# Kernel tuning notes

Measured on AMD Instinct MI355X. Metric: run time of the kernel, lower is better.

Reference implementation:

```python
import jax, jax.numpy as jnp
import numpy as np
from jax import lax

B, L, D, F, K = 16, 1024, 384, 1536, 3
MAX_DUR = 10          # clamp on per-token duration (makes output length static)
T_OUT = L * MAX_DUR   # padded expanded length
ALPHA = 1.0
EPS = 1e-5


def conv1d_same(x_ncl, w, b):
    # x_ncl: [B, Cin, L], w: [Cout, Cin, K]
    y = lax.conv_general_dilated(x_ncl, w, window_strides=(1,), padding='SAME',
                                 dimension_numbers=('NCH', 'OIH', 'NCH'))
    return y + b[None, :, None]


def conv_block(x, wA, bA, wB, bB):
    # x: [B, L, D] -> Conv(D->F) ReLU Conv(F->D) ReLU -> [B, L, D]
    h = x.transpose(0, 2, 1)
    h = jax.nn.relu(conv1d_same(h, wA, bA))
    h = jax.nn.relu(conv1d_same(h, wB, bB))
    return h.transpose(0, 2, 1)


def layernorm(x, g, b):
    mu = jnp.mean(x, axis=-1, keepdims=True)
    var = jnp.var(x, axis=-1, keepdims=True)
    return (x - mu) * lax.rsqrt(var + EPS) * g + b


def setup_inputs() -> dict:
    key = jax.random.key(0)
    ks = jax.random.split(key, 8)
    s = 0.02
    return {
        'y': jax.random.normal(ks[0], (B, L, D), jnp.float32),
        'token_lengths': jax.random.randint(ks[1], (B,), 1, L + 1).astype(jnp.int32),
        'w1a': jax.random.normal(ks[2], (F, D, K), jnp.float32) * s,
        'b1a': jnp.zeros((F,), jnp.float32),
        'w1b': jax.random.normal(ks[3], (D, F, K), jnp.float32) * s,
        'b1b': jnp.zeros((D,), jnp.float32),
        'g1': jnp.ones((D,), jnp.float32),
        'be1': jnp.zeros((D,), jnp.float32),
        'w2a': jax.random.normal(ks[4], (F, D, K), jnp.float32) * s,
        'b2a': jnp.zeros((F,), jnp.float32),
        'w2b': jax.random.normal(ks[5], (D, F, K), jnp.float32) * s,
        'b2b': jnp.zeros((D,), jnp.float32),
        'g2': jnp.ones((D,), jnp.float32),
        'be2': jnp.zeros((D,), jnp.float32),
        'wl': jax.random.normal(ks[6], (D, 1), jnp.float32) * s,
        'bl': jnp.zeros((1,), jnp.float32),
    }


def reference(y, token_lengths, w1a, b1a, w1b, b1b, g1, be1,
              w2a, b2a, w2b, b2b, g2, be2, wl, bl):
    # DurationPredictor (eval mode: dropout is identity)
    h = conv_block(y, w1a, b1a, w1b, b1b)
    h = layernorm(h, g1, be1)
    h = conv_block(h, w2a, b2a, w2b, b2b)
    h = layernorm(h, g2, be2)
    preds = h @ wl + bl                      # [B, L, 1]

    # lengths = round(alpha * exp(preds)), masked to valid tokens, clamped
    lns = jnp.round(ALPHA * jnp.exp(preds[..., 0]))
    lns = jnp.clip(lns, 0, MAX_DUR).astype(jnp.int32)        # [B, L]
    mask = jnp.arange(L)[None, :] < token_lengths[:, None]
    lns = jnp.where(mask, lns, 0)

    # ragged repeat_interleave + pad, fully vectorized:
    # output frame t maps to token idx = searchsorted(cumsum(lns), t, 'right')
    csum = jnp.cumsum(lns, axis=1)                            # [B, L]
    totals = csum[:, -1]                                      # [B]
    t = jnp.arange(T_OUT, dtype=jnp.int32)
    idx = jax.vmap(lambda c: jnp.searchsorted(c, t, side='right'))(csum)  # [B, T_OUT]
    idx = jnp.minimum(idx, L - 1)
    gathered = jnp.take_along_axis(y, idx[..., None], axis=1)  # [B, T_OUT, D]
    valid = t[None, :] < totals[:, None]
    enlarged = jnp.where(valid[..., None], gathered, 0.0)
    return enlarged, totals
```

## Files before the change

kernel.cpp:

```cpp
#include <hip/hip_runtime.h>
#include <hip/hip_bf16.h>

#define BB 16
#define LL 1024
#define DD 384
#define FF 1536
#define KK 3
#define T_OUT 10240
#define MAX_DUR 10

#define PADL 1026
#define LO_SCALE 2048.0f
#define LO_INV   4.8828125e-4f

typedef _Float16 f16x8 __attribute__((ext_vector_type(8)));
typedef float    f32x4 __attribute__((ext_vector_type(4)));

__device__ __forceinline__ void gll16(const void* g, void* l) {
    __builtin_amdgcn_global_load_lds(
        (const __attribute__((address_space(1))) void*)g,
        (__attribute__((address_space(3))) void*)l, 16, 0, 0);
}

__device__ __forceinline__ void split_write(float v, _Float16* hi, _Float16* lo, size_t off) {
    _Float16 h = (_Float16)v;
    hi[off] = h;
    lo[off] = (_Float16)((v - (float)h) * LO_SCALE);
}

__device__ __forceinline__ float split_read(const _Float16* hi, const _Float16* lo, size_t off) {
    return (float)hi[off] + (float)lo[off] * LO_INV;
}

__global__ void wfrag_k(const float* __restrict__ w, _Float16* __restrict__ hi,
                        _Float16* __restrict__ lo, int O, int I) {
    int id = blockIdx.x * 256 + threadIdx.x;
    int total = O * 3 * I;
    if (id >= total) return;
    int e = id & 7;
    int lane = (id >> 3) & 63;
    int rest = id >> 9;
    int nKT = (3 * I) >> 5;
    int ktl = rest % nKT;
    int ot = rest / nKT;
    int o = ot * 16 + (lane & 15);
    int koff = ((lane >> 4) << 3) + e;
    int kseg = ktl % 3;
    int i = (ktl / 3) * 32 + koff;
    float v = w[(o * I + i) * 3 + kseg];
    split_write(v, hi, lo, id);
}

__global__ void ysplit_k(const float* __restrict__ y, _Float16* __restrict__ hi,
                         _Float16* __restrict__ lo) {
    int id = blockIdx.x * 256 + threadIdx.x;
    if (id >= BB * PADL * DD) return;
    int d = id % DD;
    int r = id / DD;
    int b = r / PADL;
    int lr = r - b * PADL;
    float v = 0.f;
    if (lr >= 1 && lr <= LL) v = y[((size_t)(b << 10) + (lr - 1)) * DD + d];
    split_write(v, hi, lo, id);
}

__global__ void padzero_k(_Float16* __restrict__ hi, _Float16* __restrict__ lo, int width) {
    int id = blockIdx.x * 256 + threadIdx.x;
    if (id >= BB * 2 * width) return;
    int b = id / (2 * width);
    int rem = id - b * 2 * width;
    int row = (rem / width) ? (PADL - 1) : 0;
    int c = rem % width;
    size_t off = (size_t)(b * PADL + row) * width + c;
    hi[off] = (_Float16)0.f;
    lo[off] = (_Float16)0.f;
}

template<int MI, int BN, int OCC, int CIN, int COUT, int KTOT, int NN>
__global__ __launch_bounds__(256, OCC) void gemm_split(
        const _Float16* __restrict__ Ahi, const _Float16* __restrict__ Alo,
        const _Float16* __restrict__ WfH, const _Float16* __restrict__ WfL,
        const float* __restrict__ bias,
        _Float16* __restrict__ Ohi, _Float16* __restrict__ Olo) {
    constexpr int BM   = MI * 32;
    constexpr int AC   = (BM + 2) * 4;
    constexpr int AC4  = AC / 4;
    constexpr int AIT  = (AC4 + 63) / 64;
    constexpr int NA   = 2 * AIT;
    constexpr int AHH  = AC * 8;
    constexpr int ABH  = 4 * AHH;
    constexpr int SEGS = BN / 16;
    constexpr int QS   = SEGS / 4;
    constexpr int NB   = 2 * QS;
    constexpr int JJ   = BN / 32;
    constexpr int BBH  = 2 * BN * 32;
    constexpr int KEEP0  = NB;
    constexpr int KEEP12 = NA + NB;
    constexpr int nKT = KTOT >> 5;
    constexpr int nJ  = nKT / 3;
    __shared__ __align__(16) _Float16 lds_h[ABH + 2 * BBH];
    const int tid = threadIdx.x;
    const int lane = tid & 63;
    const int w = tid >> 6;
    const int lm = lane & 15, lq = lane >> 4;
    const int xcd = blockIdx.x & 7;
    const int t2 = blockIdx.x >> 3;
    const int g  = t2 / (4 * NN);
    const int r  = t2 - g * (4 * NN);
    const int n_t = r >> 2;
    const int mi  = r & 3;
    const int m_t = ((g * 4 + mi) << 3) + xcd;
    const int m0 = m_t * BM;
    const int n0 = n_t * BN;
    const int b = m0 >> 10;
    const int l0 = m0 & 1023;
    const int rowBase = b * PADL + l0;
    const int wm = (w >> 1) * (MI * 16), wn = (w & 1) * (BN / 2);

    f32x4 accM[MI][JJ], accC[MI][JJ];
    const f32x4 zz = {0.f, 0.f, 0.f, 0.f};
    #pragma unroll
    for (int i = 0; i < MI; ++i)
        #pragma unroll
        for (int jj = 0; jj < JJ; ++jj) { accM[i][jj] = zz; accC[i][jj] = zz; }

    int aRowK[AIT];
    bool aAct[AIT];
    #pragma unroll
    for (int it = 0; it < AIT; ++it) {
        int cl = it * 64 + lane;
        int s  = w * AC4 + cl;
        int p = s >> 3, sl = s & 7;
        int t = sl ^ (p & 7);
        int m = p * 2 + (t >> 2);
        int k8 = t & 3;
        aRowK[it] = (rowBase + m) * CIN + k8 * 8;
        aAct[it] = (cl < AC4);
    }
    int bBase[QS];
    #pragma unroll
    for (int q = 0; q < QS; ++q) {
        int ntg = (n0 >> 4) + w * QS + q;
        bBase[q] = (ntg * nKT * 64 + lane) * 8;
    }

    auto stageA = [&](int jt, int bidx) {
        int d0 = jt << 5;
        _Float16* abase = lds_h + bidx * (2 * AHH);
        #pragma unroll
        for (int it = 0; it < AIT; ++it) {
            size_t aoff = (size_t)(unsigned)(aRowK[it] + d0);
            _Float16* hb = abase + (w * AC4 + it * 64) * 8;
            if (aAct[it]) {
                gll16(Ahi + aoff, hb);
                gll16(Alo + aoff, hb + AHH);
            }
        }
    };

    auto stageB = [&](int kt, int bidx) {
        int ktc = kt < nKT ? kt : nKT - 1;
        _Float16* bb = lds_h + ABH + bidx * BBH;
        #pragma unroll
        for (int q = 0; q < QS; ++q) {
            int sg = w * QS + q;
            size_t boff = (size_t)(unsigned)(bBase[q] + ktc * 512);
            gll16(WfH + boff, bb + sg * 512);
            gll16(WfL + boff, bb + BN * 32 + sg * 512);
        }
    };

    auto compute = [&](const _Float16* ab, const _Float16* bb, int kseg) {
        f16x8 bH[JJ], bL[JJ];
        #pragma unroll
        for (int jj = 0; jj < JJ; ++jj) {
            int nl = (w & 1) * JJ + jj;
            bH[jj] = *(const f16x8*)(bb + nl * 512 + lane * 8);
            bL[jj] = *(const f16x8*)(bb + BN * 32 + nl * 512 + lane * 8);
        }
        __builtin_amdgcn_s_setprio(1);
        #pragma unroll
        for (int i = 0; i < MI; ++i) {
            int row = wm + i * 16 + lm + kseg;
            int p = row >> 1;
            int sl = (((row & 1) << 2) | lq) ^ (p & 7);
            int off = p * 64 + sl * 8;
            f16x8 aH = *(const f16x8*)(ab + off);
            f16x8 aL = *(const f16x8*)(ab + AHH + off);
            #pragma unroll
            for (int jj = 0; jj < JJ; ++jj) {
                accM[i][jj] = __builtin_amdgcn_mfma_f32_16x16x32_f16(aH, bH[jj], accM[i][jj], 0, 0, 0);
                accC[i][jj] = __builtin_amdgcn_mfma_f32_16x16x32_f16(aH, bL[jj], accC[i][jj], 0, 0, 0);
                accC[i][jj] = __builtin_amdgcn_mfma_f32_16x16x32_f16(aL, bH[jj], accC[i][jj], 0, 0, 0);
            }
        }
        __builtin_amdgcn_s_setprio(0);
    };

    stageB(0, 0);
    __builtin_amdgcn_sched_barrier(0);
    stageA(0, 0);
    __builtin_amdgcn_sched_barrier(0);
    stageB(1, 1);
    __builtin_amdgcn_sched_barrier(0);

    for (int j = 0; j < nJ; ++j) {
        const _Float16* ab = lds_h + (j & 1) * (2 * AHH);
        const int kt = 3 * j;
        asm volatile("s_waitcnt vmcnt(%0)" :: "i"(KEEP0) : "memory");
        __builtin_amdgcn_s_barrier();
        __builtin_amdgcn_sched_barrier(0);
        compute(ab, lds_h + ABH + (kt & 1) * BBH, 0);
        __builtin_amdgcn_sched_barrier(0);
        __builtin_amdgcn_s_barrier();
        stageB(kt + 2, kt & 1);
        __builtin_amdgcn_sched_barrier(0);
        stageA(j + 1 < nJ ? j + 1 : j, (j + 1) & 1);
        __builtin_amdgcn_sched_barrier(0);
        asm volatile("s_waitcnt vmcnt(%0)" :: "i"(KEEP12) : "memory");
        __builtin_amdgcn_s_barrier();
        __builtin_amdgcn_sched_barrier(0);
        compute(ab, lds_h + ABH + ((kt + 1) & 1) * BBH, 1);
        __builtin_amdgcn_sched_barrier(0);
        __builtin_amdgcn_s_barrier();
        stageB(kt + 3, (kt + 1) & 1);
        __builtin_amdgcn_sched_barrier(0);
        asm volatile("s_waitcnt vmcnt(%0)" :: "i"(KEEP12) : "memory");
        __builtin_amdgcn_s_barrier();
        __builtin_amdgcn_sched_barrier(0);
        compute(ab, lds_h + ABH + (kt & 1) * BBH, 2);
        __builtin_amdgcn_sched_barrier(0);
        __builtin_amdgcn_s_barrier();
        stageB(kt + 4, kt & 1);
        __builtin_amdgcn_sched_barrier(0);
    }
    #pragma unroll
    for (int i = 0; i < MI; ++i)
        #pragma unroll
        for (int jj = 0; jj < JJ; ++jj) {
            int n_g = n0 + wn + jj * 16 + lm;
            float bv = bias[n_g];
            #pragma unroll
            for (int rr = 0; rr < 4; ++rr) {
                int l = l0 + wm + i * 16 + lq * 4 + rr;
                float v = accM[i][jj][rr] + accC[i][jj][rr] * LO_INV + bv;
                v = fmaxf(v, 0.f);
                size_t off = (size_t)(b * PADL + 1 + l) * COUT + n_g;
                split_write(v, Ohi, Olo, off);
            }
        }
}

__global__ __launch_bounds__(128) void ln_split_k(
        _Float16* __restrict__ hi, _Float16* __restrict__ lo,
        const float* __restrict__ g, const float* __restrict__ be) {
    const int row = blockIdx.x;
    const int b = row >> 10, l = row & 1023;
    const size_t base = (size_t)(b * PADL + 1 + l) * DD;
    const int tid = threadIdx.x;
    float v0 = split_read(hi, lo, base + tid);
    float v1 = split_read(hi, lo, base + tid + 128);
    float v2 = split_read(hi, lo, base + tid + 256);

    __shared__ float sh[2];
    float s = v0 + v1 + v2;
    #pragma unroll
    for (int o = 32; o > 0; o >>= 1) s += __shfl_down(s, o, 64);
    if ((tid & 63) == 0) sh[tid >> 6] = s;
    __syncthreads();
    float mu = (sh[0] + sh[1]) * (1.f / DD);
    __syncthreads();
    float d0 = v0 - mu, d1 = v1 - mu, d2 = v2 - mu;
    float q = d0 * d0 + d1 * d1 + d2 * d2;
    #pragma unroll
    for (int o = 32; o > 0; o >>= 1) q += __shfl_down(q, o, 64);
    if ((tid & 63) == 0) sh[tid >> 6] = q;
    __syncthreads();
    float var = (sh[0] + sh[1]) * (1.f / DD);
    float rs = rsqrtf(var + 1e-5f);
    split_write(d0 * rs * g[tid] + be[tid], hi, lo, base + tid);
    split_write(d1 * rs * g[tid + 128] + be[tid + 128], hi, lo, base + tid + 128);
    split_write(d2 * rs * g[tid + 256] + be[tid + 256], hi, lo, base + tid + 256);
}

__global__ __launch_bounds__(128) void ln_pred_split_k(
        const _Float16* __restrict__ hi, const _Float16* __restrict__ lo,
        const float* __restrict__ g, const float* __restrict__ be,
        const float* __restrict__ wl, const float* __restrict__ bl,
        const int* __restrict__ token_lengths, int* __restrict__ lns) {
    const int row = blockIdx.x;
    const int b = row >> 10, l = row & 1023;
    const size_t base = (size_t)(b * PADL + 1 + l) * DD;
    const int tid = threadIdx.x;
    float v0 = split_read(hi, lo, base + tid);
    float v1 = split_read(hi, lo, base + tid + 128);
    float v2 = split_read(hi, lo, base + tid + 256);

    __shared__ float sh[2];
    float s = v0 + v1 + v2;
    #pragma unroll
    for (int o = 32; o > 0; o >>= 1) s += __shfl_down(s, o, 64);
    if ((tid & 63) == 0) sh[tid >> 6] = s;
    __syncthreads();
    float mu = (sh[0] + sh[1]) * (1.f / DD);
    __syncthreads();
    float d0 = v0 - mu, d1 = v1 - mu, d2 = v2 - mu;
    float q = d0 * d0 + d1 * d1 + d2 * d2;
    #pragma unroll
    for (int o = 32; o > 0; o >>= 1) q += __shfl_down(q, o, 64);
    if ((tid & 63) == 0) sh[tid >> 6] = q;
    __syncthreads();
    float var = (sh[0] + sh[1]) * (1.f / DD);
    float rs = rsqrtf(var + 1e-5f);
    __syncthreads();
    float p = (d0 * rs * g[tid]       + be[tid])       * wl[tid]
            + (d1 * rs * g[tid + 128] + be[tid + 128]) * wl[tid + 128]
            + (d2 * rs * g[tid + 256] + be[tid + 256]) * wl[tid + 256];
    #pragma unroll
    for (int o = 32; o > 0; o >>= 1) p += __shfl_down(p, o, 64);
    if ((tid & 63) == 0) sh[tid >> 6] = p;
    __syncthreads();
    if (tid == 0) {
        float pred = sh[0] + sh[1] + bl[0];
        float e = expf(pred);
        float r = rintf(e);
        r = fminf(fmaxf(r, 0.f), (float)MAX_DUR);
        int v = (int)r;
        if (l >= token_lengths[b]) v = 0;
        lns[row] = v;
    }
}

__global__ __launch_bounds__(1024) void cumsum_k(
        const int* __restrict__ lns, int* __restrict__ csum,
        float* __restrict__ totals_out) {
    __shared__ int s[1024];
    const int b = blockIdx.x, tid = threadIdx.x;
    s[tid] = lns[(b << 10) + tid];
    __syncthreads();
    #pragma unroll
    for (int o = 1; o < 1024; o <<= 1) {
        int t = (tid >= o) ? s[tid - o] : 0;
        __syncthreads();
        s[tid] += t;
        __syncthreads();
    }
    csum[(b << 10) + tid] = s[tid];
    if (tid == 1023) totals_out[b] = (float)s[1023];
}

__global__ __launch_bounds__(256) void gather_k(
        const float* __restrict__ y, const int* __restrict__ csum,
        float* __restrict__ out) {
    int gid = blockIdx.x * 256 + threadIdx.x;
    int c4 = gid % 96;
    int rest = gid / 96;
    int t = rest % T_OUT;
    int b = rest / T_OUT;
    const int* c = csum + (b << 10);
    int total = c[1023];
    float4 r = make_float4(0.f, 0.f, 0.f, 0.f);
    if (t < total) {
        int lo = 0, hi = 1024;
        while (lo < hi) {
            int mid = (lo + hi) >> 1;
            if (c[mid] <= t) lo = mid + 1; else hi = mid;
        }
        int idx = min(lo, LL - 1);
        r = *(const float4*)(y + ((size_t)((b << 10) + idx)) * DD + (c4 << 2));
    }
    *(float4*)(out + ((size_t)b * T_OUT + t) * DD + (c4 << 2)) = r;
}

extern "C" void kernel_launch(void* const* d_in, const int* in_sizes, int n_in,
                              void* d_out, int out_size, void* d_ws, size_t ws_size,
                              hipStream_t stream) {
    const float* y   = (const float*)d_in[0];
    const int*   tok = (const int*)d_in[1];
    const float* w1a = (const float*)d_in[2];
    const float* b1a = (const float*)d_in[3];
    const float* w1b = (const float*)d_in[4];
    const float* b1b = (const float*)d_in[5];
    const float* g1  = (const float*)d_in[6];
    const float* be1 = (const float*)d_in[7];
    const float* w2a = (const float*)d_in[8];
    const float* b2a = (const float*)d_in[9];
    const float* w2b = (const float*)d_in[10];
    const float* b2b = (const float*)d_in[11];
    const float* g2  = (const float*)d_in[12];
    const float* be2 = (const float*)d_in[13];
    const float* wl  = (const float*)d_in[14];
    const float* bl  = (const float*)d_in[15];

    float* out = (float*)d_out;

    const size_t WN   = (size_t)FF * DD * KK;
    const size_t SN   = (size_t)BB * PADL * DD;
    const size_t H1N  = (size_t)BB * PADL * FF;
    _Float16* p = (_Float16*)d_ws;
    _Float16* Wh1a = p;              _Float16* Wl1a = Wh1a + WN;
    _Float16* Wh1b = Wl1a + WN;      _Float16* Wl1b = Wh1b + WN;
    _Float16* Wh2a = Wl1b + WN;      _Float16* Wl2a = Wh2a + WN;
    _Float16* Wh2b = Wl2a + WN;      _Float16* Wl2b = Wh2b + WN;
    _Float16* Shi  = Wl2b + WN;      _Float16* Slo  = Shi + SN;
    _Float16* H1hi = Slo + SN;       _Float16* H1lo = H1hi + H1N;
    int* lns  = (int*)(H1lo + H1N);
    int* csum = lns + BB * LL;

    const int M = BB * LL;

    {
        int n = FF * DD * KK;
        wfrag_k<<<(n + 255) / 256, 256, 0, stream>>>(w1a, Wh1a, Wl1a, FF, DD);
        wfrag_k<<<(n + 255) / 256, 256, 0, stream>>>(w1b, Wh1b, Wl1b, DD, FF);
        wfrag_k<<<(n + 255) / 256, 256, 0, stream>>>(w2a, Wh2a, Wl2a, FF, DD);
        wfrag_k<<<(n + 255) / 256, 256, 0, stream>>>(w2b, Wh2b, Wl2b, DD, FF);
        int ny = BB * PADL * DD;
        ysplit_k<<<(ny + 255) / 256, 256, 0, stream>>>(y, Shi, Slo);
        int np = BB * 2 * FF;
        padzero_k<<<(np + 255) / 256, 256, 0, stream>>>(H1hi, H1lo, FF);
    }
    gemm_split<4, 64, 3, DD, FF, 3 * DD, FF / 64>
        <<<(FF / 64) * (M / 128), 256, 0, stream>>>(Shi, Slo, Wh1a, Wl1a, b1a, H1hi, H1lo);
    gemm_split<4, 64, 3, FF, DD, 3 * FF, DD / 64>
        <<<(DD / 64) * (M / 128), 256, 0, stream>>>(H1hi, H1lo, Wh1b, Wl1b, b1b, Shi, Slo);
    ln_split_k<<<M, 128, 0, stream>>>(Shi, Slo, g1, be1);
    gemm_split<4, 64, 3, DD, FF, 3 * DD, FF / 64>
        <<<(FF / 64) * (M / 128), 256, 0, stream>>>(Shi, Slo, Wh2a, Wl2a, b2a, H1hi, H1lo);
    gemm_split<4, 64, 3, FF, DD, 3 * FF, DD / 64>
        <<<(DD / 64) * (M / 128), 256, 0, stream>>>(H1hi, H1lo, Wh2b, Wl2b, b2b, Shi, Slo);
    ln_pred_split_k<<<M, 128, 0, stream>>>(Shi, Slo, g2, be2, wl, bl, tok, lns);
    cumsum_k<<<BB, 1024, 0, stream>>>(lns, csum, out + (size_t)BB * T_OUT * DD);
    {
        long long n = (long long)BB * T_OUT * 96;
        gather_k<<<(int)((n + 255) / 256), 256, 0, stream>>>(y, csum, out);
    }
}
```

Baseline: 993.0 us.

## Restructure conv GEMM pipeline: load all three taps' weights per step, widen N tile

The conv-as-GEMM kernel now stages the B fragments for all three kernel taps of a k-block at once into a single LDS buffer. It pulls them into registers, then issues the next global-to-LDS loads before running the MFMA chain. A-fragment LDS reads are software-pipelined one step ahead, and the N tile grows from 64 to 96 with launch bounds occupancy set to 2. This cuts the barriers per k-block from six to two and raises reuse of each A tile. The cost is higher register pressure, single-buffered B with a full vmcnt(0) wait each iteration, and lower occupancy.

```diff
diff --git a/kernel.cpp b/kernel.cpp
--- a/kernel.cpp
+++ b/kernel.cpp
@@ -76,8 +76,8 @@
     lo[off] = (_Float16)0.f;
 }
 
-template<int MI, int BN, int OCC, int CIN, int COUT, int KTOT, int NN>
-__global__ __launch_bounds__(256, OCC) void gemm_split(
+template<int MI, int BN, int CIN, int COUT, int KTOT, int NN>
+__global__ __launch_bounds__(256, 2) void gemm_fused(
         const _Float16* __restrict__ Ahi, const _Float16* __restrict__ Alo,
         const _Float16* __restrict__ WfH, const _Float16* __restrict__ WfL,
         const float* __restrict__ bias,
@@ -86,19 +86,15 @@
     constexpr int AC   = (BM + 2) * 4;
     constexpr int AC4  = AC / 4;
     constexpr int AIT  = (AC4 + 63) / 64;
-    constexpr int NA   = 2 * AIT;
     constexpr int AHH  = AC * 8;
     constexpr int ABH  = 4 * AHH;
     constexpr int SEGS = BN / 16;
-    constexpr int QS   = SEGS / 4;
-    constexpr int NB   = 2 * QS;
     constexpr int JJ   = BN / 32;
-    constexpr int BBH  = 2 * BN * 32;
-    constexpr int KEEP0  = NB;
-    constexpr int KEEP12 = NA + NB;
+    constexpr int BHALF = 3 * SEGS * 512;
+    constexpr int BUNITS = 3 * SEGS;
     constexpr int nKT = KTOT >> 5;
     constexpr int nJ  = nKT / 3;
-    __shared__ __align__(16) _Float16 lds_h[ABH + 2 * BBH];
+    __shared__ __align__(16) _Float16 lds_h[ABH + 2 * BHALF];
     const int tid = threadIdx.x;
     const int lane = tid & 63;
     const int w = tid >> 6;
@@ -137,11 +133,25 @@
         aRowK[it] = (rowBase + m) * CIN + k8 * 8;
         aAct[it] = (cl < AC4);
     }
-    int bBase[QS];
-    #pragma unroll
-    for (int q = 0; q < QS; ++q) {
-        int ntg = (n0 >> 4) + w * QS + q;
-        bBase[q] = (ntg * nKT * 64 + lane) * 8;
+    int bOffK[5];
+    int bDstH[5];
+    bool bActv[5];
+    #pragma unroll
+    for (int t = 0; t < 5; ++t) {
+        int u = w + 4 * t;
+        bActv[t] = (u < BUNITS);
+        int uc = bActv[t] ? u : 0;
+        int s = uc / SEGS, seg = uc % SEGS;
+        bOffK[t] = (((n0 >> 4) + seg) * nKT * 64 + lane) * 8 + s * 512;
+        bDstH[t] = uc * 512;
+    }
+    int aOff[MI * 3];
+    #pragma unroll
+    for (int t = 0; t < MI * 3; ++t) {
+        int row = wm + (t & 3) * 16 + lm + (t >> 2);
+        int p = row >> 1;
+        int sl = (((row & 1) << 2) | lq) ^ (p & 7);
+        aOff[t] = p * 64 + sl * 8;
     }
 
     auto stageA = [&](int jt, int bidx) {
@@ -158,80 +168,67 @@
         }
     };
 
-    auto stageB = [&](int kt, int bidx) {
-        int ktc = kt < nKT ? kt : nKT - 1;
-        _Float16* bb = lds_h + ABH + bidx * BBH;
+    auto stageB = [&](int jt) {
+        int jc = jt < nJ ? jt : nJ - 1;
+        _Float16* bb = lds_h + ABH;
         #pragma unroll
-        for (int q = 0; q < QS; ++q) {
-            int sg = w * QS + q;
-            size_t boff = (size_t)(unsigned)(bBase[q] + ktc * 512);
-            gll16(WfH + boff, bb + sg * 512);
-            gll16(WfL + boff, bb + BN * 32 + sg * 512);
+        for (int t = 0; t < 5; ++t) {
+            if (bActv[t]) {
+                size_t boff = (size_t)(unsigned)(bOffK[t] + jc * 1536);
+                gll16(WfH + boff, bb + bDstH[t]);
+                gll16(WfL + boff, bb + BHALF + bDstH[t]);
+            }
         }
     };
 
-    auto compute = [&](const _Float16* ab, const _Float16* bb, int kseg) {
-        f16x8 bH[JJ], bL[JJ];
+    stageB(0);
+    stageA(0, 0);
+
+    for (int j = 0; j < nJ; ++j) {
+        asm volatile("s_waitcnt vmcnt(0)" ::: "memory");
+        __builtin_amdgcn_s_barrier();
+        __builtin_amdgcn_sched_barrier(0);
+        f16x8 bH[3][JJ], bL[3][JJ];
+        {
+            const _Float16* bb = lds_h + ABH;
+            #pragma unroll
+            for (int s = 0; s < 3; ++s)
+                #pragma unroll
+                for (int jj = 0; jj < JJ; ++jj) {
+                    int nl = (w & 1) * JJ + jj;
+                    const _Float16* pB = bb + (s * SEGS + nl) * 512 + lane * 8;
+                    bH[s][jj] = *(const f16x8*)pB;
+                    bL[s][jj] = *(const f16x8*)(pB + BHALF);
+                }
+        }
+        __builtin_amdgcn_sched_barrier(0);
+        asm volatile("s_waitcnt lgkmcnt(0)" ::: "memory");
+        __builtin_amdgcn_s_barrier();
+        __builtin_amdgcn_sched_barrier(0);
+        stageB(j + 1);
+        stageA(j + 1 < nJ ? j + 1 : nJ - 1, (j + 1) & 1);
+        __builtin_amdgcn_sched_barrier(0);
+        const _Float16* ab = lds_h + (j & 1) * (2 * AHH);
+        __builtin_amdgcn_s_setprio(1);
+        f16x8 aHc = *(const f16x8*)(ab + aOff[0]);
+        f16x8 aLc = *(const f16x8*)(ab + AHH + aOff[0]);
         #pragma unroll
-        for (int jj = 0; jj < JJ; ++jj) {
-            int nl = (w & 1) * JJ + jj;
-            bH[jj] = *(const f16x8*)(bb + nl * 512 + lane * 8);
-            bL[jj] = *(const f16x8*)(bb + BN * 32 + nl * 512 + lane * 8);
-        }
-        __builtin_amdgcn_s_setprio(1);
-        #pragma unroll
-        for (int i = 0; i < MI; ++i) {
-            int row = wm + i * 16 + lm + kseg;
-            int p = row >> 1;
-            int sl = (((row & 1) << 2) | lq) ^ (p & 7);
-            int off = p * 64 + sl * 8;
-            f16x8 aH = *(const f16x8*)(ab + off);
-            f16x8 aL = *(const f16x8*)(ab + AHH + off);
+        for (int t = 0; t < MI * 3; ++t) {
+            f16x8 aHn, aLn;
+            if (t < MI * 3 - 1) {
+                aHn = *(const f16x8*)(ab + aOff[t + 1]);
+                aLn = *(const f16x8*)(ab + AHH + aOff[t + 1]);
+            }
+            int s = t >> 2, i = t & 3;
             #pragma unroll
             for (int jj = 0; jj < JJ; ++jj) {
-                accM[i][jj] = __builtin_amdgcn_mfma_f32_16x16x32_f16(aH, bH[jj], accM[i][jj], 0, 0, 0);
-                accC[i][jj] = __builtin_amdgcn_mfma_f32_16x16x32_f16(aH, bL[jj], accC[i][jj], 0, 0, 0);
-                accC[i][jj] = __builtin_amdgcn_mfma_f32_16x16x32_f16(aL, bH[jj], accC[i][jj], 0, 0, 0);
+                accM[i][jj] = __builtin_amdgcn_mfma_f32_16x16x32_f16(aHc, bH[s][jj], accM[i][jj], 0, 0, 0);
+                accC[i][jj] = __builtin_amdgcn_mfma_f32_16x16x32_f16(aHc, bL[s][jj], accC[i][jj], 0, 0, 0);
+                accC[i][jj] = __builtin_amdgcn_mfma_f32_16x16x32_f16(aLc, bH[s][jj], accC[i][jj], 0, 0, 0);
             }
+            aHc = aHn; aLc = aLn;
         }
         __builtin_amdgcn_s_setprio(0);
-    };
-
-    stageB(0, 0);
-    __builtin_amdgcn_sched_barrier(0);
-    stageA(0, 0);
-    __builtin_amdgcn_sched_barrier(0);
-    stageB(1, 1);
-    __builtin_amdgcn_sched_barrier(0);
-
-    for (int j = 0; j < nJ; ++j) {
-        const _Float16* ab = lds_h + (j & 1) * (2 * AHH);
-        const int kt = 3 * j;
-        asm volatile("s_waitcnt vmcnt(%0)" :: "i"(KEEP0) : "memory");
-        __builtin_amdgcn_s_barrier();
-        __builtin_amdgcn_sched_barrier(0);
-        compute(ab, lds_h + ABH + (kt & 1) * BBH, 0);
-        __builtin_amdgcn_sched_barrier(0);
-        __builtin_amdgcn_s_barrier();
-        stageB(kt + 2, kt & 1);
-        __builtin_amdgcn_sched_barrier(0);
-        stageA(j + 1 < nJ ? j + 1 : j, (j + 1) & 1);
-        __builtin_amdgcn_sched_barrier(0);
-        asm volatile("s_waitcnt vmcnt(%0)" :: "i"(KEEP12) : "memory");
-        __builtin_amdgcn_s_barrier();
-        __builtin_amdgcn_sched_barrier(0);
-        compute(ab, lds_h + ABH + ((kt + 1) & 1) * BBH, 1);
-        __builtin_amdgcn_sched_barrier(0);
-        __builtin_amdgcn_s_barrier();
-        stageB(kt + 3, (kt + 1) & 1);
-        __builtin_amdgcn_sched_barrier(0);
-        asm volatile("s_waitcnt vmcnt(%0)" :: "i"(KEEP12) : "memory");
-        __builtin_amdgcn_s_barrier();
-        __builtin_amdgcn_sched_barrier(0);
-        compute(ab, lds_h + ABH + (kt & 1) * BBH, 2);
-        __builtin_amdgcn_sched_barrier(0);
-        __builtin_amdgcn_s_barrier();
-        stageB(kt + 4, kt & 1);
         __builtin_amdgcn_sched_barrier(0);
     }
     #pragma unroll
@@ -420,15 +417,15 @@
         int np = BB * 2 * FF;
         padzero_k<<<(np + 255) / 256, 256, 0, stream>>>(H1hi, H1lo, FF);
     }
-    gemm_split<4, 64, 3, DD, FF, 3 * DD, FF / 64>
-        <<<(FF / 64) * (M / 128), 256, 0, stream>>>(Shi, Slo, Wh1a, Wl1a, b1a, H1hi, H1lo);
-    gemm_split<4, 64, 3, FF, DD, 3 * FF, DD / 64>
-        <<<(DD / 64) * (M / 128), 256, 0, stream>>>(H1hi, H1lo, Wh1b, Wl1b, b1b, Shi, Slo);
+    gemm_fused<4, 96, DD, FF, 3 * DD, FF / 96>
+        <<<(FF / 96) * (M / 128), 256, 0, stream>>>(Shi, Slo, Wh1a, Wl1a, b1a, H1hi, H1lo);
+    gemm_fused<4, 96, FF, DD, 3 * FF, DD / 96>
+        <<<(DD / 96) * (M / 128), 256, 0, stream>>>(H1hi, H1lo, Wh1b, Wl1b, b1b, Shi, Slo);
     ln_split_k<<<M, 128, 0, stream>>>(Shi, Slo, g1, be1);
-    gemm_split<4, 64, 3, DD, FF, 3 * DD, FF / 64>
-        <<<(FF / 64) * (M / 128), 256, 0, stream>>>(Shi, Slo, Wh2a, Wl2a, b2a, H1hi, H1lo);
-    gemm_split<4, 64, 3, FF, DD, 3 * FF, DD / 64>
-        <<<(DD / 64) * (M / 128), 256, 0, stream>>>(H1hi, H1lo, Wh2b, Wl2b, b2b, Shi, Slo);
+    gemm_fused<4, 96, DD, FF, 3 * DD, FF / 96>
+        <<<(FF / 96) * (M / 128), 256, 0, stream>>>(Shi, Slo, Wh2a, Wl2a, b2a, H1hi, H1lo);
+    gemm_fused<4, 96, FF, DD, 3 * FF, DD / 96>
+        <<<(DD / 96) * (M / 128), 256, 0, stream>>>(H1hi, H1lo, Wh2b, Wl2b, b2b, Shi, Slo);
     ln_pred_split_k<<<M, 128, 0, stream>>>(Shi, Slo, g2, be2, wl, bl, tok, lns);
     cumsum_k<<<BB, 1024, 0, stream>>>(lns, csum, out + (size_t)BB * T_OUT * DD);
     {
```

Result: faster. 952.6 us (-4.1%).

## Load GEMM weight fragments directly into registers instead of staging through LDS

Applied to the files above, without the earlier changes.

The split-fp16 conv-GEMM kernel no longer stages the weight (B) fragments through shared memory. Each wave now loads its own two weight fragments straight from global memory into registers, double-buffered across K-steps, while only the activation tile stays in LDS. This removes most per-step barriers and LDS traffic for B, and the LDS row offsets are now precomputed. In exchange, each wave issues duplicate global loads for weights that were shared before, which adds register pressure and relies on L2 to serve the repeated weight reads.

```diff
diff --git a/kernel.cpp b/kernel.cpp
--- a/kernel.cpp
+++ b/kernel.cpp
@@ -76,29 +76,20 @@
     lo[off] = (_Float16)0.f;
 }
 
-template<int MI, int BN, int OCC, int CIN, int COUT, int KTOT, int NN>
-__global__ __launch_bounds__(256, OCC) void gemm_split(
+template<int CIN, int COUT, int KTOT, int NN>
+__global__ __launch_bounds__(256, 3) void gemm_breg(
         const _Float16* __restrict__ Ahi, const _Float16* __restrict__ Alo,
         const _Float16* __restrict__ WfH, const _Float16* __restrict__ WfL,
         const float* __restrict__ bias,
         _Float16* __restrict__ Ohi, _Float16* __restrict__ Olo) {
-    constexpr int BM   = MI * 32;
+    constexpr int BM   = 128;
     constexpr int AC   = (BM + 2) * 4;
     constexpr int AC4  = AC / 4;
     constexpr int AIT  = (AC4 + 63) / 64;
-    constexpr int NA   = 2 * AIT;
     constexpr int AHH  = AC * 8;
-    constexpr int ABH  = 4 * AHH;
-    constexpr int SEGS = BN / 16;
-    constexpr int QS   = SEGS / 4;
-    constexpr int NB   = 2 * QS;
-    constexpr int JJ   = BN / 32;
-    constexpr int BBH  = 2 * BN * 32;
-    constexpr int KEEP0  = NB;
-    constexpr int KEEP12 = NA + NB;
-    constexpr int nKT = KTOT >> 5;
-    constexpr int nJ  = nKT / 3;
-    __shared__ __align__(16) _Float16 lds_h[ABH + 2 * BBH];
+    constexpr int nKT  = KTOT >> 5;
+    constexpr int nJ   = nKT / 3;
+    __shared__ __align__(16) _Float16 lds_h[4 * AHH];
     const int tid = threadIdx.x;
     const int lane = tid & 63;
     const int w = tid >> 6;
@@ -111,18 +102,18 @@
     const int mi  = r & 3;
     const int m_t = ((g * 4 + mi) << 3) + xcd;
     const int m0 = m_t * BM;
-    const int n0 = n_t * BN;
+    const int n0 = n_t * 64;
     const int b = m0 >> 10;
     const int l0 = m0 & 1023;
     const int rowBase = b * PADL + l0;
-    const int wm = (w >> 1) * (MI * 16), wn = (w & 1) * (BN / 2);
-
-    f32x4 accM[MI][JJ], accC[MI][JJ];
+    const int wm = (w >> 1) * 64, wn = (w & 1) * 32;
+
+    f32x4 accM[4][2], accC[4][2];
     const f32x4 zz = {0.f, 0.f, 0.f, 0.f};
     #pragma unroll
-    for (int i = 0; i < MI; ++i)
+    for (int i = 0; i < 4; ++i)
         #pragma unroll
-        for (int jj = 0; jj < JJ; ++jj) { accM[i][jj] = zz; accC[i][jj] = zz; }
+        for (int jj = 0; jj < 2; ++jj) { accM[i][jj] = zz; accC[i][jj] = zz; }
 
     int aRowK[AIT];
     bool aAct[AIT];
@@ -137,11 +128,19 @@
         aRowK[it] = (rowBase + m) * CIN + k8 * 8;
         aAct[it] = (cl < AC4);
     }
-    int bBase[QS];
-    #pragma unroll
-    for (int q = 0; q < QS; ++q) {
-        int ntg = (n0 >> 4) + w * QS + q;
-        bBase[q] = (ntg * nKT * 64 + lane) * 8;
+    int baseB[2];
+    #pragma unroll
+    for (int jj = 0; jj < 2; ++jj) {
+        int ntg = (n0 >> 4) + (w & 1) * 2 + jj;
+        baseB[jj] = (ntg * nKT * 64 + lane) * 8;
+    }
+    int aOff[12];
+    #pragma unroll
+    for (int t = 0; t < 12; ++t) {
+        int row = wm + (t & 3) * 16 + lm + (t >> 2);
+        int p = row >> 1;
+        int sl = (((row & 1) << 2) | lq) ^ (p & 7);
+        aOff[t] = p * 64 + sl * 8;
     }
 
     auto stageA = [&](int jt, int bidx) {
@@ -158,86 +157,94 @@
         }
     };
 
-    auto stageB = [&](int kt, int bidx) {
-        int ktc = kt < nKT ? kt : nKT - 1;
-        _Float16* bb = lds_h + ABH + bidx * BBH;
+    auto loadB = [&](int p, f16x8* dH, f16x8* dL) {
+        int pc = p < nKT ? p : nKT - 1;
         #pragma unroll
-        for (int q = 0; q < QS; ++q) {
-            int sg = w * QS + q;
-            size_t boff = (size_t)(unsigned)(bBase[q] + ktc * 512);
-            gll16(WfH + boff, bb + sg * 512);
-            gll16(WfL + boff, bb + BN * 32 + sg * 512);
+        for (int jj = 0; jj < 2; ++jj) {
+            size_t off = (size_t)(unsigned)(baseB[jj] + pc * 512);
+            dH[jj] = *(const f16x8*)(WfH + off);
+            dL[jj] = *(const f16x8*)(WfL + off);
         }
     };
 
-    auto compute = [&](const _Float16* ab, const _Float16* bb, int kseg) {
-        f16x8 bH[JJ], bL[JJ];
-        #pragma unroll
-        for (int jj = 0; jj < JJ; ++jj) {
-            int nl = (w & 1) * JJ + jj;
-            bH[jj] = *(const f16x8*)(bb + nl * 512 + lane * 8);
-            bL[jj] = *(const f16x8*)(bb + BN * 32 + nl * 512 + lane * 8);
-        }
+    auto compute = [&](const _Float16* ab, int s, const f16x8* bh, const f16x8* bl) {
         __builtin_amdgcn_s_setprio(1);
         #pragma unroll
-        for (int i = 0; i < MI; ++i) {
-            int row = wm + i * 16 + lm + kseg;
-            int p = row >> 1;
-            int sl = (((row & 1) << 2) | lq) ^ (p & 7);
-            int off = p * 64 + sl * 8;
+        for (int i = 0; i < 4; ++i) {
+            int off = aOff[s * 4 + i];
             f16x8 aH = *(const f16x8*)(ab + off);
             f16x8 aL = *(const f16x8*)(ab + AHH + off);
             #pragma unroll
-            for (int jj = 0; jj < JJ; ++jj) {
-                accM[i][jj] = __builtin_amdgcn_mfma_f32_16x16x32_f16(aH, bH[jj], accM[i][jj], 0, 0, 0);
-                accC[i][jj] = __builtin_amdgcn_mfma_f32_16x16x32_f16(aH, bL[jj], accC[i][jj], 0, 0, 0);
-                accC[i][jj] = __builtin_amdgcn_mfma_f32_16x16x32_f16(aL, bH[jj], accC[i][jj], 0, 0, 0);
+            for (int jj = 0; jj < 2; ++jj) {
+                accM[i][jj] = __builtin_amdgcn_mfma_f32_16x16x32_f16(aH, bh[jj], accM[i][jj], 0, 0, 0);
+                accC[i][jj] = __builtin_amdgcn_mfma_f32_16x16x32_f16(aH, bl[jj], accC[i][jj], 0, 0, 0);
+                accC[i][jj] = __builtin_amdgcn_mfma_f32_16x16x32_f16(aL, bh[jj], accC[i][jj], 0, 0, 0);
             }
         }
         __builtin_amdgcn_s_setprio(0);
     };
 
-    stageB(0, 0);
-    __builtin_amdgcn_sched_barrier(0);
+    f16x8 b0H[2], b0L[2], b1H[2], b1L[2];
     stageA(0, 0);
     __builtin_amdgcn_sched_barrier(0);
-    stageB(1, 1);
+    loadB(0, b0H, b0L);
     __builtin_amdgcn_sched_barrier(0);
-
-    for (int j = 0; j < nJ; ++j) {
-        const _Float16* ab = lds_h + (j & 1) * (2 * AHH);
-        const int kt = 3 * j;
-        asm volatile("s_waitcnt vmcnt(%0)" :: "i"(KEEP0) : "memory");
+    asm volatile("s_waitcnt vmcnt(4)" ::: "memory");
+    __builtin_amdgcn_s_barrier();
+
+    for (int jm = 0; jm < nJ; jm += 2) {
+        const _Float16* bufE = lds_h;
+        const _Float16* bufO = lds_h + 2 * AHH;
+        const int p0 = 3 * jm;
+        loadB(p0 + 1, b1H, b1L);
+        stageA(jm + 1 < nJ ? jm + 1 : nJ - 1, 1);
+        __builtin_amdgcn_sched_barrier(0);
+        asm volatile("s_waitcnt vmcnt(10)" ::: "memory");
+        __builtin_amdgcn_sched_barrier(0);
+        compute(bufE, 0, b0H, b0L);
+        __builtin_amdgcn_sched_barrier(0);
+
+        loadB(p0 + 2, b0H, b0L);
+        __builtin_amdgcn_sched_barrier(0);
+        asm volatile("s_waitcnt vmcnt(10)" ::: "memory");
+        __builtin_amdgcn_sched_barrier(0);
+        compute(bufE, 1, b1H, b1L);
+        __builtin_amdgcn_sched_barrier(0);
+
+        loadB(p0 + 3, b1H, b1L);
+        __builtin_amdgcn_sched_barrier(0);
+        asm volatile("s_waitcnt vmcnt(4)" ::: "memory");
+        __builtin_amdgcn_sched_barrier(0);
+        compute(bufE, 2, b0H, b0L);
+        __builtin_amdgcn_sched_barrier(0);
         __builtin_amdgcn_s_barrier();
-        __builtin_amdgcn_sched_barrier(0);
-        compute(ab, lds_h + ABH + (kt & 1) * BBH, 0);
+        loadB(p0 + 4, b0H, b0L);
+        stageA(jm + 2 < nJ ? jm + 2 : nJ - 1, 0);
+        __builtin_amdgcn_sched_barrier(0);
+        asm volatile("s_waitcnt vmcnt(10)" ::: "memory");
+        __builtin_amdgcn_sched_barrier(0);
+        compute(bufO, 0, b1H, b1L);
+        __builtin_amdgcn_sched_barrier(0);
+
+        loadB(p0 + 5, b1H, b1L);
+        __builtin_amdgcn_sched_barrier(0);
+        asm volatile("s_waitcnt vmcnt(10)" ::: "memory");
+        __builtin_amdgcn_sched_barrier(0);
+        compute(bufO, 1, b0H, b0L);
+        __builtin_amdgcn_sched_barrier(0);
+
+        loadB(p0 + 6, b0H, b0L);
+        __builtin_amdgcn_sched_barrier(0);
+        asm volatile("s_waitcnt vmcnt(4)" ::: "memory");
+        __builtin_amdgcn_sched_barrier(0);
+        compute(bufO, 2, b1H, b1L);
         __builtin_amdgcn_sched_barrier(0);
         __builtin_amdgcn_s_barrier();
-        stageB(kt + 2, kt & 1);
-        __builtin_amdgcn_sched_barrier(0);
-        stageA(j + 1 < nJ ? j + 1 : j, (j + 1) & 1);
-        __builtin_amdgcn_sched_barrier(0);
-        asm volatile("s_waitcnt vmcnt(%0)" :: "i"(KEEP12) : "memory");
-        __builtin_amdgcn_s_barrier();
-        __builtin_amdgcn_sched_barrier(0);
-        compute(ab, lds_h + ABH + ((kt + 1) & 1) * BBH, 1);
-        __builtin_amdgcn_sched_barrier(0);
-        __builtin_amdgcn_s_barrier();
-        stageB(kt + 3, (kt + 1) & 1);
-        __builtin_amdgcn_sched_barrier(0);
-        asm volatile("s_waitcnt vmcnt(%0)" :: "i"(KEEP12) : "memory");
-        __builtin_amdgcn_s_barrier();
-        __builtin_amdgcn_sched_barrier(0);
-        compute(ab, lds_h + ABH + (kt & 1) * BBH, 2);
-        __builtin_amdgcn_sched_barrier(0);
-        __builtin_amdgcn_s_barrier();
-        stageB(kt + 4, kt & 1);
-        __builtin_amdgcn_sched_barrier(0);
-    }
-    #pragma unroll
-    for (int i = 0; i < MI; ++i)
+    }
+    #pragma unroll
+    for (int i = 0; i < 4; ++i)
         #pragma unroll
-        for (int jj = 0; jj < JJ; ++jj) {
+        for (int jj = 0; jj < 2; ++jj) {
             int n_g = n0 + wn + jj * 16 + lm;
             float bv = bias[n_g];
             #pragma unroll
@@ -420,14 +427,14 @@
         int np = BB * 2 * FF;
         padzero_k<<<(np + 255) / 256, 256, 0, stream>>>(H1hi, H1lo, FF);
     }
-    gemm_split<4, 64, 3, DD, FF, 3 * DD, FF / 64>
+    gemm_breg<DD, FF, 3 * DD, FF / 64>
         <<<(FF / 64) * (M / 128), 256, 0, stream>>>(Shi, Slo, Wh1a, Wl1a, b1a, H1hi, H1lo);
-    gemm_split<4, 64, 3, FF, DD, 3 * FF, DD / 64>
+    gemm_breg<FF, DD, 3 * FF, DD / 64>
         <<<(DD / 64) * (M / 128), 256, 0, stream>>>(H1hi, H1lo, Wh1b, Wl1b, b1b, Shi, Slo);
     ln_split_k<<<M, 128, 0, stream>>>(Shi, Slo, g1, be1);
-    gemm_split<4, 64, 3, DD, FF, 3 * DD, FF / 64>
+    gemm_breg<DD, FF, 3 * DD, FF / 64>
         <<<(FF / 64) * (M / 128), 256, 0, stream>>>(Shi, Slo, Wh2a, Wl2a, b2a, H1hi, H1lo);
-    gemm_split<4, 64, 3, FF, DD, 3 * FF, DD / 64>
+    gemm_breg<FF, DD, 3 * FF, DD / 64>
         <<<(DD / 64) * (M / 128), 256, 0, stream>>>(H1hi, H1lo, Wh2b, Wl2b, b2b, Shi, Slo);
     ln_pred_split_k<<<M, 128, 0, stream>>>(Shi, Slo, g2, be2, wl, bl, tok, lns);
     cumsum_k<<<BB, 1024, 0, stream>>>(lns, csum, out + (size_t)BB * T_OUT * DD);
```

Measured after the change: 983.6 us. No clear change (-0.9%).
